# Kernel optimization log

Hardware: AMD Instinct MI355X
Metric: run time of the kernel (lower is better)

Reference implementation:

```python
import jax, jax.numpy as jnp
import numpy as np
from jax import lax

B, T, H, L, LAT, OUT, NH = 4096, 60, 512, 2, 128, 14, 4
EPS = 1e-5


def _ln(x, g, b):
    m = x.mean(-1, keepdims=True)
    v = ((x - m) ** 2).mean(-1, keepdims=True)
    return (x - m) / jnp.sqrt(v + EPS) * g + b


def setup_inputs() -> dict:
    key = jax.random.key(0)
    ks = jax.random.split(key, 24)
    f32 = jnp.float32
    def rn(k, shape, s=0.05):
        return jax.random.normal(k, shape, dtype=f32) * s
    return {
        'x': jax.random.normal(ks[0], (B, T, 17), dtype=f32),
        'conv1_w': rn(ks[1], (24, 9, 3)), 'conv1_b': rn(ks[2], (24,)),
        'bn1_g': jnp.ones(24, f32), 'bn1_b': jnp.zeros(24, f32),
        'bn1_rm': rn(ks[3], (24,), 0.1), 'bn1_rv': jnp.full((24,), 0.8, f32),
        'comp_w': rn(ks[4], (20, 8)), 'comp_b': rn(ks[5], (20,)),
        'proj_w': rn(ks[6], (H, 44)), 'proj_b': rn(ks[7], (H,)),
        'gates_w': rn(ks[8], (L, 5, H, 2 * H), 0.02), 'gates_b': rn(ks[9], (L, 5, H)),
        'retention': jnp.full((L, H), 0.9, f32),
        'expln_g': jnp.ones((L, H), f32), 'expln_b': jnp.zeros((L, H), f32),
        'ln_g': jnp.ones((L, H), f32), 'ln_b': jnp.zeros((L, H), f32),
        'attn_in_w': rn(ks[10], (3 * H, H), 0.02), 'attn_in_b': rn(ks[11], (3 * H,)),
        'attn_out_w': rn(ks[12], (H, H), 0.02), 'attn_out_b': rn(ks[13], (H,)),
        'bneck_w': rn(ks[14], (LAT, H)), 'bneck_b': rn(ks[15], (LAT,)),
        'bn2_g': jnp.ones(LAT, f32), 'bn2_b': jnp.zeros(LAT, f32),
        'bn2_rm': rn(ks[16], (LAT,), 0.1), 'bn2_rv': jnp.full((LAT,), 0.9, f32),
        'out_w': rn(ks[17], (OUT, LAT)), 'out_b': rn(ks[18], (OUT,)),
    }


def _forward(x, conv1_w, conv1_b, bn1_g, bn1_b, bn1_rm, bn1_rv, comp_w, comp_b,
             proj_w, proj_b, gates_w, gates_b, retention, expln_g, expln_b,
             ln_g, ln_b, attn_in_w, attn_in_b, attn_out_w, attn_out_b,
             bneck_w, bneck_b, bn2_g, bn2_b, bn2_rm, bn2_rv, out_w, out_b):
    bsz = x.shape[0]
    hd = proj_w.shape[0]
    nlayers = gates_w.shape[0]
    # --- conv branch on relative features (eval-mode BatchNorm) ---
    rel = x[:, :, :9].transpose(0, 2, 1)                      # [B,9,T]
    y = lax.conv_general_dilated(rel, conv1_w, (1,), [(1, 1)],
                                 dimension_numbers=('NCH', 'OIH', 'NCH'))
    y = jax.nn.relu(y + conv1_b[None, :, None])
    y = (y - bn1_rm[None, :, None]) / jnp.sqrt(bn1_rv + EPS)[None, :, None] \
        * bn1_g[None, :, None] + bn1_b[None, :, None]
    th = y.shape[2] // 2
    y = y[:, :, :th * 2].reshape(bsz, 24, th, 2).max(-1)      # MaxPool1d(2)
    rel_feat = y.transpose(0, 2, 1)                           # [B,30,24]
    # --- company embedding branch ---
    comp = jax.nn.relu(x[:, :30, 9:] @ comp_w.T + comp_b)     # [B,30,20]
    combined = jnp.concatenate([rel_feat, comp], -1) @ proj_w.T + proj_b  # [B,30,H]
    # --- stacked xLSTM over time ---
    h0 = jnp.zeros((nlayers, bsz, hd), x.dtype)
    c0 = jnp.zeros((nlayers, bsz, hd), x.dtype)
    def step(carry, x_t):
        h, c = carry
        inp = x_t
        hs, cs = [], []
        for l in range(nlayers):
            comb = jnp.concatenate([inp, h[l]], -1)           # [B,2H]
            g = jnp.einsum('bk,ghk->gbh', comb, gates_w[l]) + gates_b[l][:, None, :]
            f = jax.nn.sigmoid(g[0]); i = jax.nn.sigmoid(g[1])
            o = jax.nn.sigmoid(g[2]); cc = jnp.tanh(g[3]); m = jax.nn.sigmoid(g[4])
            r = retention[l]
            c_new = f * c[l] + i * cc
            c_new = c_new * r + (1 - r) * c[l]
            c_new = m * c_new + (1 - m) * c[l]
            o_exp = jax.nn.sigmoid(_ln(o, expln_g[l], expln_b[l]))  # exp(z)/(1+exp(z))
            h_new = _ln(o_exp * jnp.tanh(c_new), ln_g[l], ln_b[l])
            hs.append(h_new); cs.append(c_new)
            inp = h_new
        return (jnp.stack(hs), jnp.stack(cs)), inp
    _, seq = lax.scan(step, (h0, c0), combined.transpose(1, 0, 2))
    seq = seq.transpose(1, 0, 2)                              # [B,30,H]
    # --- multi-head self attention (eval, 4 heads) ---
    dh = hd // NH
    qkv = seq @ attn_in_w.T + attn_in_b
    q, k, v = jnp.split(qkv, 3, axis=-1)
    q = q.reshape(bsz, -1, NH, dh); k = k.reshape(bsz, -1, NH, dh); v = v.reshape(bsz, -1, NH, dh)
    scores = jnp.einsum('bqhd,bkhd->bhqk', q, k) / jnp.sqrt(jnp.float32(dh))
    attn = jnp.einsum('bhqk,bkhd->bqhd', jax.nn.softmax(scores, -1), v)
    attn = attn.reshape(bsz, -1, hd) @ attn_out_w.T + attn_out_b
    final = attn[:, -1, :]
    latent = final @ bneck_w.T + bneck_b
    latent = (latent - bn2_rm) / jnp.sqrt(bn2_rv + EPS) * bn2_g + bn2_b
    return latent @ out_w.T + out_b


def reference(x, conv1_w, conv1_b, bn1_g, bn1_b, bn1_rm, bn1_rv, comp_w, comp_b,
              proj_w, proj_b, gates_w, gates_b, retention, expln_g, expln_b,
              ln_g, ln_b, attn_in_w, attn_in_b, attn_out_w, attn_out_b,
              bneck_w, bneck_b, bn2_g, bn2_b, bn2_rm, bn2_rv, out_w, out_b):
    return _forward(x, conv1_w, conv1_b, bn1_g, bn1_b, bn1_rm, bn1_rv, comp_w, comp_b,
                    proj_w, proj_b, gates_w, gates_b, retention, expln_g, expln_b,
                    ln_g, ln_b, attn_in_w, attn_in_b, attn_out_w, attn_out_b,
                    bneck_w, bneck_b, bn2_g, bn2_b, bn2_rm, bn2_rv, out_w, out_b)
```

## Files before the change

kernel.cpp:

```cpp
#include <hip/hip_runtime.h>
#include <hip/hip_bf16.h>

#define B_   4096
#define T_   60
#define TT   30
#define H_   512
#define L_   2
#define NH_  4
#define DH_  128
#define LAT_ 128
#define OUT_ 14
#define NGATE_ (5*H_)
#define EPSF 1e-5f
#define FEATK 64
#define K0M  (FEATK + H_)

typedef __attribute__((ext_vector_type(8))) short bf16x8;
typedef __attribute__((ext_vector_type(4))) short bf16x4;
typedef __attribute__((ext_vector_type(4))) float f32x4;

__device__ __forceinline__ float sigmoidf_(float x) { return 1.0f / (1.0f + __expf(-x)); }
__device__ __forceinline__ float bf2f(short s) {
    return __uint_as_float(((unsigned)(unsigned short)s) << 16);
}

__device__ __forceinline__ void async_load16(const void* g, void* l) {
    __builtin_amdgcn_global_load_lds((const __attribute__((address_space(1))) void*)g,
                                     (__attribute__((address_space(3))) void*)l, 16, 0, 0);
}

__device__ __forceinline__ int perm_row(int n) {
    int g = n >> 9, j = n & 511;
    return (j >> 4) * 80 + g * 16 + (j & 15);
}

__global__ __launch_bounds__(256) void cvt_bf16(const float* __restrict__ in,
                                                __hip_bfloat16* __restrict__ out, long n) {
    long i = (long)blockIdx.x * blockDim.x + threadIdx.x;
    long stride = (long)gridDim.x * blockDim.x;
    for (; i < n; i += stride) out[i] = __float2bfloat16(in[i]);
}

__global__ __launch_bounds__(256) void zero_f32(float* __restrict__ p, long n) {
    long i = (long)blockIdx.x * blockDim.x + threadIdx.x;
    long stride = (long)gridDim.x * blockDim.x;
    for (; i < n; i += stride) p[i] = 0.0f;
}

__global__ __launch_bounds__(256)
void perm_w1(const float* __restrict__ gw, __hip_bfloat16* __restrict__ w1p) {
    long i = (long)blockIdx.x * 256 + threadIdx.x;
    if (i >= (long)NGATE_ * 2 * H_) return;
    int n = (int)(i >> 10), k = (int)(i & 1023);
    w1p[(long)perm_row(n) * (2 * H_) + k] = __float2bfloat16(gw[i]);
}

__global__ __launch_bounds__(256)
void build_w0m(const float* __restrict__ gw, const float* __restrict__ pw,
               const float* __restrict__ pb, const float* __restrict__ gb,
               __hip_bfloat16* __restrict__ w0p, float* __restrict__ bc) {
    const int tid = threadIdx.x;
    const int n = blockIdx.x * 4 + (tid >> 6);
    const int f = tid & 63;
    const long np = perm_row(n);
    const float* wrow = gw + (long)n * (2 * H_);
    float acc = 0.f;
    if (f < 44) {
        for (int k = 0; k < H_; ++k) acc += wrow[k] * pw[k * 44 + f];
    }
    w0p[np * K0M + f] = __float2bfloat16(acc);
    #pragma unroll
    for (int j = 0; j < 8; ++j) {
        int col = f * 8 + j;
        w0p[np * K0M + FEATK + col] = __float2bfloat16(wrow[H_ + col]);
    }
    float s = 0.f;
    #pragma unroll
    for (int j = 0; j < 8; ++j) s += wrow[f * 8 + j] * pb[f * 8 + j];
    #pragma unroll
    for (int off = 32; off > 0; off >>= 1) s += __shfl_down(s, off, 64);
    if (f == 0) bc[n] = gb[n] + s;
}

__global__ __launch_bounds__(256)
void build_wkd(const float* __restrict__ aiw, __hip_bfloat16* __restrict__ wkd) {
    int i = blockIdx.x * 256 + threadIdx.x;
    if (i >= 2048 * 512) return;
    int n = i >> 9, k = i & 511;
    float v = ((k >> 7) == (n >> 9)) ? aiw[(H_ + k) * H_ + (n & 511)] : 0.f;
    wkd[i] = __float2bfloat16(v);
}

__global__ __launch_bounds__(256)
void build_wvd(const float* __restrict__ aiw, __hip_bfloat16* __restrict__ wvd) {
    int i = blockIdx.x * 256 + threadIdx.x;
    if (i >= 512 * 2048) return;
    int n = i >> 11, k = i & 2047;
    float v = ((k >> 9) == (n >> 7)) ? aiw[(2 * H_ + n) * H_ + (k & 511)] : 0.f;
    wvd[i] = __float2bfloat16(v);
}

__global__ __launch_bounds__(256)
void frontend_kernel(const float* __restrict__ x,
                     const float* __restrict__ cw, const float* __restrict__ cb,
                     const float* __restrict__ bg, const float* __restrict__ bb,
                     const float* __restrict__ brm, const float* __restrict__ brv,
                     const float* __restrict__ compw, const float* __restrict__ compb,
                     __hip_bfloat16* __restrict__ feat_out) {
    const int b = blockIdx.x, tid = threadIdx.x;
    __shared__ float xs[T_ * 17];
    __shared__ float ybuf[24][T_];
    __shared__ float feat[TT][44];

    for (int i = tid; i < T_ * 17; i += 256) xs[i] = x[(long)b * T_ * 17 + i];
    __syncthreads();

    for (int i = tid; i < 24 * T_; i += 256) {
        int oc = i / T_, t = i % T_;
        float acc = cb[oc];
        #pragma unroll
        for (int kk = 0; kk < 3; ++kk) {
            int tt = t + kk - 1;
            if (tt >= 0 && tt < T_) {
                #pragma unroll
                for (int ic = 0; ic < 9; ++ic)
                    acc += xs[tt * 17 + ic] * cw[(oc * 9 + ic) * 3 + kk];
            }
        }
        acc = fmaxf(acc, 0.f);
        acc = (acc - brm[oc]) * rsqrtf(brv[oc] + EPSF) * bg[oc] + bb[oc];
        ybuf[oc][t] = acc;
    }
    __syncthreads();

    for (int i = tid; i < TT * 24; i += 256) {
        int u = i / 24, oc = i % 24;
        feat[u][oc] = fmaxf(ybuf[oc][2 * u], ybuf[oc][2 * u + 1]);
    }
    for (int i = tid; i < TT * 20; i += 256) {
        int u = i / 20, oc = i % 20;
        float acc = compb[oc];
        #pragma unroll
        for (int j = 0; j < 8; ++j) acc += xs[u * 17 + 9 + j] * compw[oc * 8 + j];
        feat[u][24 + oc] = fmaxf(acc, 0.f);
    }
    __syncthreads();

    for (int i = tid; i < TT * FEATK; i += 256) {
        int u = i >> 6, c = i & 63;
        float v = (c < 44) ? feat[u][c] : 0.f;
        feat_out[((long)b * TT + u) * FEATK + c] = __float2bfloat16(v);
    }
}

template <int WRITE_BF16>
__device__ __forceinline__
void gemm_core(const __hip_bfloat16* __restrict__ A0, int lda0,
               const __hip_bfloat16* __restrict__ A1, int lda1, int ksplit,
               const __hip_bfloat16* __restrict__ W, int ldw,
               const float* __restrict__ bias,
               void* __restrict__ Cout, int ldc, int K, int bx, int by) {
    __shared__ __hip_bfloat16 As[128 * 64];
    __shared__ __hip_bfloat16 Bs[128 * 64];
    const int tid = threadIdx.x;
    const int wave = tid >> 6, lane = tid & 63;
    const long m0 = (long)by * 128;
    const long n0 = (long)bx * 128;

    f32x4 acc[4][4] = {};

    for (int k0 = 0; k0 < K; k0 += 64) {
        __syncthreads();
        #pragma unroll
        for (int it = 0; it < 4; ++it) {
            int id = it * 256 + tid;
            int row = id >> 3;
            int kc = ((id & 7) ^ (row & 7)) << 3;
            int gk = k0 + kc;
            const __hip_bfloat16* srcA;
            if (gk < ksplit) srcA = A0 + (m0 + row) * (long)lda0 + gk;
            else             srcA = A1 + (m0 + row) * (long)lda1 + (gk - ksplit);
            async_load16(srcA, &As[id * 8]);
            const __hip_bfloat16* srcB = W + (n0 + row) * (long)ldw + gk;
            async_load16(srcB, &Bs[id * 8]);
        }
        __syncthreads();
        #pragma unroll
        for (int ks = 0; ks < 2; ++ks) {
            const int kb = ((ks * 4 + (lane >> 4)) ^ (lane & 7)) << 3;
            const int ar = (wave >> 1) * 64 + (lane & 15);
            const int br = (wave & 1) * 64 + (lane & 15);
            bf16x8 afr[4], bfr[4];
            #pragma unroll
            for (int i = 0; i < 4; ++i) afr[i] = *(const bf16x8*)&As[(ar + i * 16) * 64 + kb];
            #pragma unroll
            for (int i = 0; i < 4; ++i) bfr[i] = *(const bf16x8*)&Bs[(br + i * 16) * 64 + kb];
            #pragma unroll
            for (int mi = 0; mi < 4; ++mi)
                #pragma unroll
                for (int ni = 0; ni < 4; ++ni)
                    acc[mi][ni] = __builtin_amdgcn_mfma_f32_16x16x32_bf16(afr[mi], bfr[ni], acc[mi][ni], 0, 0, 0);
        }
    }

    const int cr = (lane >> 4) * 4;
    const int ccol = lane & 15;
    #pragma unroll
    for (int ni = 0; ni < 4; ++ni) {
        long col = n0 + (wave & 1) * 64 + ni * 16 + ccol;
        float bv = bias ? bias[col] : 0.f;
        #pragma unroll
        for (int mi = 0; mi < 4; ++mi) {
            long rowb = m0 + (wave >> 1) * 64 + mi * 16 + cr;
            #pragma unroll
            for (int r = 0; r < 4; ++r) {
                float v = acc[mi][ni][r] + bv;
                if (WRITE_BF16)
                    ((__hip_bfloat16*)Cout)[(rowb + r) * (long)ldc + col] = __float2bfloat16(v);
                else
                    ((float*)Cout)[(rowb + r) * (long)ldc + col] = v;
            }
        }
    }
}

template <int WRITE_BF16>
__global__ __launch_bounds__(256)
void gemm_bias(const __hip_bfloat16* __restrict__ A0, int lda0,
               const __hip_bfloat16* __restrict__ A1, int lda1, int ksplit,
               const __hip_bfloat16* __restrict__ W, int ldw,
               const float* __restrict__ bias,
               void* __restrict__ Cout, int ldc, int K) {
    gemm_core<WRITE_BF16>(A0, lda0, A1, lda1, ksplit, W, ldw, bias, Cout, ldc, K,
                          blockIdx.x, blockIdx.y);
}

__device__ __forceinline__
void fused_gate_core(const __hip_bfloat16* __restrict__ A0, int lda0,
                     const __hip_bfloat16* __restrict__ A1, int lda1,
                     int ksplit, int K,
                     const __hip_bfloat16* __restrict__ Wp, int ldw,
                     const float* __restrict__ bias,
                     const float* __restrict__ ret,
                     float* __restrict__ c_t,
                     float* __restrict__ opre,
                     float* __restrict__ tcn,
                     int m, int nblk) {
    __shared__ __hip_bfloat16 As[2][128 * 32];
    __shared__ __hip_bfloat16 Bs[2][80 * 32];
    const int tid = threadIdx.x;
    const int wave = tid >> 6, lane = tid & 63;
    const long m0 = (long)m * 128;
    const int n0row = nblk * 80;
    const int jbase = nblk * 16;

    f32x4 acc[2][5] = {};

    auto stage = [&](int hb, int k0) {
        #pragma unroll
        for (int it = 0; it < 2; ++it) {
            int sid = it * 256 + tid;
            int row = sid >> 2;
            int kc = ((sid & 3) ^ ((row >> 1) & 3)) << 3;
            int gk = k0 + kc;
            const __hip_bfloat16* srcA;
            if (gk < ksplit) srcA = A0 + (m0 + row) * (long)lda0 + gk;
            else             srcA = A1 + (m0 + row) * (long)lda1 + (gk - ksplit);
            async_load16(srcA, &As[hb][sid * 8]);
        }
        {
            int sid = tid;
            int row = sid >> 2;
            int kc = ((sid & 3) ^ ((row >> 1) & 3)) << 3;
            async_load16(Wp + (long)(n0row + row) * ldw + k0 + kc, &Bs[hb][sid * 8]);
        }
        if (tid < 64) {
            int sid = 256 + tid;
            int row = sid >> 2;
            int kc = ((sid & 3) ^ ((row >> 1) & 3)) << 3;
            async_load16(Wp + (long)(n0row + row) * ldw + k0 + kc, &Bs[hb][sid * 8]);
        }
    };

    stage(0, 0);
    const int nslab = K >> 5;
    const int kb = ((lane >> 4) ^ ((lane >> 1) & 3)) << 3;
    const int arb = wave * 32 + (lane & 15);
    const int brb = lane & 15;

    for (int kk = 0; kk < nslab; ++kk) {
        const int hb = kk & 1;
        __syncthreads();
        if (kk + 1 < nslab) stage(hb ^ 1, (kk + 1) << 5);
        bf16x8 afr[2], bfr[5];
        #pragma unroll
        for (int i = 0; i < 2; ++i) afr[i] = *(const bf16x8*)&As[hb][(arb + i * 16) * 32 + kb];
        #pragma unroll
        for (int i = 0; i < 5; ++i) bfr[i] = *(const bf16x8*)&Bs[hb][(brb + i * 16) * 32 + kb];
        #pragma unroll
        for (int mi = 0; mi < 2; ++mi)
            #pragma unroll
            for (int ni = 0; ni < 5; ++ni)
                acc[mi][ni] = __builtin_amdgcn_mfma_f32_16x16x32_bf16(bfr[ni], afr[mi], acc[mi][ni], 0, 0, 0);
    }

    const int q = lane >> 4;
    #pragma unroll
    for (int mi = 0; mi < 2; ++mi) {
        const long b = m0 + wave * 32 + mi * 16 + (lane & 15);
        f32x4 ov, tv;
        #pragma unroll
        for (int r = 0; r < 4; ++r) {
            const int jg = jbase + 4 * q + r;
            float f  = sigmoidf_(acc[mi][0][r] + bias[jg]);
            float ii = sigmoidf_(acc[mi][1][r] + bias[512 + jg]);
            float o  = sigmoidf_(acc[mi][2][r] + bias[1024 + jg]);
            float cc = tanhf(acc[mi][3][r] + bias[1536 + jg]);
            float mg = sigmoidf_(acc[mi][4][r] + bias[2048 + jg]);
            float cold = c_t[(long)jg * B_ + b];
            float rr = ret[jg];
            float cn = f * cold + ii * cc;
            cn = cn * rr + (1.f - rr) * cold;
            cn = mg * cn + (1.f - mg) * cold;
            c_t[(long)jg * B_ + b] = cn;
            ov[r] = o;
            tv[r] = tanhf(cn);
        }
        *(f32x4*)&opre[b * H_ + jbase + 4 * q] = ov;
        *(f32x4*)&tcn [b * H_ + jbase + 4 * q] = tv;
    }
}

__global__ __launch_bounds__(256)
void fused_gate_single(const __hip_bfloat16* A0, int lda0, const __hip_bfloat16* A1,
                       int lda1, int ksplit, int K,
                       const __hip_bfloat16* Wp, int ldw,
                       const float* bias, const float* ret, float* c_t,
                       float* opre, float* tcn) {
    const int id = blockIdx.x;
    const int xcd = id & 7;
    const int rest = id >> 3;
    const int m = xcd * 4 + (rest & 3);
    const int n = (rest >> 2) & 31;
    fused_gate_core(A0, lda0, A1, lda1, ksplit, K, Wp, ldw, bias, ret, c_t,
                    opre, tcn, m, n);
}

__global__ __launch_bounds__(256)
void fused_gate_dual(const __hip_bfloat16* A0a, int lda0a, const __hip_bfloat16* A1a,
                     int lda1a, int ksplita, int Ka,
                     const __hip_bfloat16* Wpa, int ldwa,
                     const float* biasa, const float* reta, float* cta,
                     float* oprea, float* tcna,
                     const __hip_bfloat16* A0b, int lda0b, const __hip_bfloat16* A1b,
                     int lda1b, int ksplitb, int Kb,
                     const __hip_bfloat16* Wpb, int ldwb,
                     const float* biasb, const float* retb, float* ctb,
                     float* opreb, float* tcnb) {
    const int id = blockIdx.x;
    const int xcd = id & 7;
    const int rest = id >> 3;
    const int m = xcd * 4 + (rest & 3);
    const int n = (rest >> 2) & 31;
    const int z = rest >> 7;
    if (z == 0)
        fused_gate_core(A0a, lda0a, A1a, lda1a, ksplita, Ka, Wpa, ldwa,
                        biasa, reta, cta, oprea, tcna, m, n);
    else
        fused_gate_core(A0b, lda0b, A1b, lda1b, ksplitb, Kb, Wpb, ldwb,
                        biasb, retb, ctb, opreb, tcnb, m, n);
}

__device__ __forceinline__ void block_reduce2(float& a, float& b, float* red) {
    #pragma unroll
    for (int off = 32; off > 0; off >>= 1) {
        a += __shfl_down(a, off, 64);
        b += __shfl_down(b, off, 64);
    }
    int lane = threadIdx.x & 63, w = threadIdx.x >> 6;
    if (lane == 0) { red[w] = a; red[8 + w] = b; }
    __syncthreads();
    a = red[0] + red[1] + red[2] + red[3];
    b = red[8] + red[9] + red[10] + red[11];
    __syncthreads();
}

__device__ __forceinline__
void gate_ln_body(const float* __restrict__ opre,
                  const float* __restrict__ tcn,
                  const float* __restrict__ elg, const float* __restrict__ elb,
                  const float* __restrict__ lng, const float* __restrict__ lnb,
                  __hip_bfloat16* __restrict__ hout, long hstride, int b) {
    const int tid = threadIdx.x;
    __shared__ float red[16];

    float o_[2], t_[2];
    float s = 0.f, s2 = 0.f;
    #pragma unroll
    for (int u = 0; u < 2; ++u) {
        int j = tid + u * 256;
        float o = opre[(long)b * H_ + j];
        float t = tcn[(long)b * H_ + j];
        o_[u] = o; t_[u] = t;
        s += o; s2 += o * o;
    }
    block_reduce2(s, s2, red);
    float mean = s * (1.f / H_);
    float var = s2 * (1.f / H_) - mean * mean;
    float rstd = rsqrtf(var + EPSF);

    float val[2];
    float s3 = 0.f, s4 = 0.f;
    #pragma unroll
    for (int u = 0; u < 2; ++u) {
        int j = tid + u * 256;
        float on = (o_[u] - mean) * rstd * elg[j] + elb[j];
        float v = sigmoidf_(on) * t_[u];
        val[u] = v; s3 += v; s4 += v * v;
    }
    block_reduce2(s3, s4, red);
    float mean2 = s3 * (1.f / H_);
    float var2 = s4 * (1.f / H_) - mean2 * mean2;
    float rstd2 = rsqrtf(var2 + EPSF);
    #pragma unroll
    for (int u = 0; u < 2; ++u) {
        int j = tid + u * 256;
        float h = (val[u] - mean2) * rstd2 * lng[j] + lnb[j];
        hout[(long)b * hstride + j] = __float2bfloat16(h);
    }
}

__global__ __launch_bounds__(256)
void gate_ln(const float* __restrict__ opre,
             const float* __restrict__ tcn,
             const float* __restrict__ elg, const float* __restrict__ elb,
             const float* __restrict__ lng, const float* __restrict__ lnb,
             __hip_bfloat16* __restrict__ hout, long hstride) {
    gate_ln_body(opre, tcn, elg, elb, lng, lnb, hout, hstride, blockIdx.x);
}

__global__ __launch_bounds__(256)
void gate_ln_dual(const float* oa, const float* ta,
                  const float* elga, const float* elba,
                  const float* lnga, const float* lnba,
                  __hip_bfloat16* houta, long hstridea,
                  const float* ob, const float* tb,
                  const float* elgb, const float* elbb,
                  const float* lngb, const float* lnbb,
                  __hip_bfloat16* houtb, long hstrideb) {
    int bid = blockIdx.x;
    bool isB = bid >= B_;
    int b = isB ? bid - B_ : bid;
    gate_ln_body(isB ? ob : oa, isB ? tb : ta,
                 isB ? elgb : elga, isB ? elbb : elba,
                 isB ? lngb : lnga, isB ? lnbb : lnba,
                 isB ? houtb : houta, isB ? hstrideb : hstridea, b);
}

__global__ __launch_bounds__(256)
void attn_fused(const __hip_bfloat16* __restrict__ seq,
                const __hip_bfloat16* __restrict__ U,
                __hip_bfloat16* __restrict__ sbar) {
    const int b = blockIdx.x, tid = threadIdx.x;
    const int h = tid >> 6, lane = tid & 63;
    const int c0 = lane * 8;
    __shared__ float ps[NH_ * TT];
    const float scale = 0.08838834764831845f;

    float uq[8];
    {
        bf16x8 uv = *(const bf16x8*)&U[(size_t)b * (NH_ * H_) + h * H_ + c0];
        for (int j = 0; j < 8; ++j) uq[j] = bf2f(uv[j]);
    }
    const __hip_bfloat16* srow = seq + (size_t)b * TT * H_;

    for (int t = 0; t < TT; ++t) {
        bf16x8 sv = *(const bf16x8*)&srow[t * H_ + c0];
        float a = 0.f;
        for (int j = 0; j < 8; ++j) a += uq[j] * bf2f(sv[j]);
        a += __shfl_xor(a, 32);
        a += __shfl_xor(a, 16);
        a += __shfl_xor(a, 8);
        a += __shfl_xor(a, 4);
        a += __shfl_xor(a, 2);
        a += __shfl_xor(a, 1);
        if (lane == 0) ps[h * TT + t] = a * scale;
    }
    __syncthreads();

    float mx = -1e30f;
    for (int t = 0; t < TT; ++t) mx = fmaxf(mx, ps[h * TT + t]);
    float den = 0.f;
    for (int t = 0; t < TT; ++t) den += __expf(ps[h * TT + t] - mx);
    float inv = 1.f / den;

    float accv[8];
    for (int j = 0; j < 8; ++j) accv[j] = 0.f;
    for (int t = 0; t < TT; ++t) {
        float w = __expf(ps[h * TT + t] - mx) * inv;
        bf16x8 sv = *(const bf16x8*)&srow[t * H_ + c0];
        for (int j = 0; j < 8; ++j) accv[j] += w * bf2f(sv[j]);
    }
    bf16x8 outv;
    for (int j = 0; j < 8; ++j) {
        __hip_bfloat16 hv = __float2bfloat16(accv[j]);
        outv[j] = *(short*)&hv;
    }
    *(bf16x8*)&sbar[(size_t)b * (NH_ * H_) + h * H_ + c0] = outv;
}

__global__ __launch_bounds__(128)
void head_kernel(const float* __restrict__ lat_in,
                 const float* __restrict__ g2, const float* __restrict__ b2,
                 const float* __restrict__ rm2, const float* __restrict__ rv2,
                 const float* __restrict__ ow, const float* __restrict__ ob,
                 float* __restrict__ out) {
    const int b = blockIdx.x, tid = threadIdx.x;
    __shared__ float ls[LAT_];
    float a = lat_in[(long)b * LAT_ + tid];
    ls[tid] = (a - rm2[tid]) * rsqrtf(rv2[tid] + EPSF) * g2[tid] + b2[tid];
    __syncthreads();
    if (tid < OUT_) {
        float acc = ob[tid];
        #pragma unroll 4
        for (int j = 0; j < LAT_; ++j) acc += ls[j] * ow[tid * LAT_ + j];
        out[(long)b * OUT_ + tid] = acc;
    }
}

extern "C" void kernel_launch(void* const* d_in, const int* in_sizes, int n_in,
                              void* d_out, int out_size, void* d_ws, size_t ws_size,
                              hipStream_t stream) {
    const float* x        = (const float*)d_in[0];
    const float* conv1_w  = (const float*)d_in[1];
    const float* conv1_b  = (const float*)d_in[2];
    const float* bn1_g    = (const float*)d_in[3];
    const float* bn1_b    = (const float*)d_in[4];
    const float* bn1_rm   = (const float*)d_in[5];
    const float* bn1_rv   = (const float*)d_in[6];
    const float* comp_w   = (const float*)d_in[7];
    const float* comp_b   = (const float*)d_in[8];
    const float* proj_w   = (const float*)d_in[9];
    const float* proj_b   = (const float*)d_in[10];
    const float* gates_w  = (const float*)d_in[11];
    const float* gates_b  = (const float*)d_in[12];
    const float* retention= (const float*)d_in[13];
    const float* expln_g  = (const float*)d_in[14];
    const float* expln_b  = (const float*)d_in[15];
    const float* ln_g     = (const float*)d_in[16];
    const float* ln_b     = (const float*)d_in[17];
    const float* attn_in_w  = (const float*)d_in[18];
    const float* attn_in_b  = (const float*)d_in[19];
    const float* attn_out_w = (const float*)d_in[20];
    const float* attn_out_b = (const float*)d_in[21];
    const float* bneck_w  = (const float*)d_in[22];
    const float* bneck_b  = (const float*)d_in[23];
    const float* bn2_g    = (const float*)d_in[24];
    const float* bn2_b    = (const float*)d_in[25];
    const float* bn2_rm   = (const float*)d_in[26];
    const float* bn2_rv   = (const float*)d_in[27];
    const float* out_w    = (const float*)d_in[28];
    const float* out_b    = (const float*)d_in[29];
    float* out = (float*)d_out;

    char* base = (char*)d_ws;
    size_t off = 0;
    auto alloc = [&](size_t nbytes) -> char* {
        char* p = base + off;
        off += (nbytes + 255) & ~(size_t)255;
        return p;
    };
    __hip_bfloat16* seq_bf = (__hip_bfloat16*)alloc((size_t)B_ * TT * H_ * 2);
    size_t g_bytes = (size_t)B_ * NGATE_ * 2;
    char* un = alloc(2 * g_bytes);
    float* opreA = (float*)un;
    float* tcnA  = (float*)(un + (size_t)8 * 1024 * 1024);
    float* opreB = (float*)(un + (size_t)16 * 1024 * 1024);
    float* tcnB  = (float*)(un + (size_t)24 * 1024 * 1024);
    __hip_bfloat16* U_bf    = (__hip_bfloat16*)un;
    __hip_bfloat16* sbar_bf = (__hip_bfloat16*)(un + (size_t)16 * 1024 * 1024);
    __hip_bfloat16* wkd_bf  = (__hip_bfloat16*)(un + (size_t)32 * 1024 * 1024);
    __hip_bfloat16* wvd_bf  = (__hip_bfloat16*)(un + (size_t)35 * 1024 * 1024);
    __hip_bfloat16* feat_bf = (__hip_bfloat16*)alloc((size_t)B_ * TT * FEATK * 2);
    float*          c0t   = (float*)alloc((size_t)B_ * H_ * 4);
    float*          c1t   = (float*)alloc((size_t)B_ * H_ * 4);
    __hip_bfloat16* h0_bf = (__hip_bfloat16*)alloc((size_t)B_ * H_ * 2);
    __hip_bfloat16* q_bf  = (__hip_bfloat16*)alloc((size_t)B_ * H_ * 2);
    __hip_bfloat16* fin_bf = q_bf;
    __hip_bfloat16* av_bf = (__hip_bfloat16*)alloc((size_t)B_ * H_ * 2);
    float*          lat_f = (float*)alloc((size_t)B_ * LAT_ * 4);
    __hip_bfloat16* w1p_bf = (__hip_bfloat16*)alloc((size_t)NGATE_ * 2 * H_ * 2);
    __hip_bfloat16* w0p_bf = (__hip_bfloat16*)alloc((size_t)NGATE_ * K0M * 2);
    float*          bc_f  = (float*)alloc((size_t)NGATE_ * 4);
    __hip_bfloat16* ai_bf = (__hip_bfloat16*)alloc((size_t)H_ * H_ * 2);
    __hip_bfloat16* ao_bf = (__hip_bfloat16*)alloc((size_t)H_ * H_ * 2);
    __hip_bfloat16* bw_bf = (__hip_bfloat16*)alloc((size_t)LAT_ * H_ * 2);
    (void)ws_size; (void)in_sizes; (void)n_in; (void)out_size;

    const int WL = 5 * H_ * 2 * H_;
    perm_w1<<<(NGATE_ * 2 * H_) / 256, 256, 0, stream>>>(gates_w + WL, w1p_bf);
    build_w0m<<<NGATE_ / 4, 256, 0, stream>>>(gates_w, proj_w, proj_b, gates_b,
                                              w0p_bf, bc_f);
    cvt_bf16<<<256, 256, 0, stream>>>(attn_in_w, ai_bf, (long)H_ * H_);
    cvt_bf16<<<256, 256, 0, stream>>>(attn_out_w, ao_bf, (long)H_ * H_);
    cvt_bf16<<<64, 256, 0, stream>>>(bneck_w, bw_bf, (long)LAT_ * H_);
    zero_f32<<<2048, 256, 0, stream>>>(c0t, (long)2 * B_ * H_);

    frontend_kernel<<<B_, 256, 0, stream>>>(x, conv1_w, conv1_b, bn1_g, bn1_b, bn1_rm,
                                            bn1_rv, comp_w, comp_b, feat_bf);

    fused_gate_single<<<1024, 256, 0, stream>>>(
        feat_bf, TT * FEATK, (const __hip_bfloat16*)nullptr, 0, FEATK, FEATK,
        w0p_bf, K0M, bc_f, retention, c0t, opreB, tcnB);
    gate_ln<<<B_, 256, 0, stream>>>(opreB, tcnB, expln_g, expln_b,
                                    ln_g, ln_b, h0_bf, H_);

    for (int t = 0; t < TT - 1; ++t) {
        fused_gate_dual<<<2048, 256, 0, stream>>>(
            h0_bf, H_, (t == 0) ? (const __hip_bfloat16*)nullptr
                                : seq_bf + (size_t)(t - 1) * H_,
            TT * H_, H_, (t == 0) ? H_ : 2 * H_,
            w1p_bf, 2 * H_, gates_b + NGATE_, retention + H_, c1t, opreA, tcnA,
            feat_bf + (size_t)(t + 1) * FEATK, TT * FEATK, h0_bf, H_, FEATK, K0M,
            w0p_bf, K0M, bc_f, retention, c0t, opreB, tcnB);
        gate_ln_dual<<<2 * B_, 256, 0, stream>>>(
            opreA, tcnA, expln_g + H_, expln_b + H_, ln_g + H_, ln_b + H_,
            seq_bf + (size_t)t * H_, TT * H_,
            opreB, tcnB, expln_g, expln_b, ln_g, ln_b, h0_bf, H_);
    }
    fused_gate_single<<<1024, 256, 0, stream>>>(
        h0_bf, H_, seq_bf + (size_t)(TT - 2) * H_, TT * H_, H_, 2 * H_,
        w1p_bf, 2 * H_, gates_b + NGATE_, retention + H_, c1t, opreA, tcnA);
    gate_ln<<<B_, 256, 0, stream>>>(opreA, tcnA, expln_g + H_, expln_b + H_,
                                    ln_g + H_, ln_b + H_,
                                    seq_bf + (size_t)(TT - 1) * H_, TT * H_);

    build_wkd<<<4096, 256, 0, stream>>>(attn_in_w, wkd_bf);
    build_wvd<<<4096, 256, 0, stream>>>(attn_in_w, wvd_bf);

    gemm_bias<1><<<dim3(H_ / 128, B_ / 128), 256, 0, stream>>>(
        seq_bf + (size_t)29 * H_, TT * H_, (const __hip_bfloat16*)nullptr, 0, H_,
        ai_bf, H_, attn_in_b, (void*)q_bf, H_, H_);

    gemm_bias<1><<<dim3(2048 / 128, B_ / 128), 256, 0, stream>>>(
        q_bf, H_, (const __hip_bfloat16*)nullptr, 0, H_,
        wkd_bf, H_, (const float*)nullptr, (void*)U_bf, 2048, H_);

    attn_fused<<<B_, 256, 0, stream>>>(seq_bf, U_bf, sbar_bf);

    gemm_bias<1><<<dim3(H_ / 128, B_ / 128), 256, 0, stream>>>(
        sbar_bf, 2048, (const __hip_bfloat16*)nullptr, 0, 2048,
        wvd_bf, 2048, attn_in_b + 2 * H_, (void*)av_bf, H_, 2048);

    gemm_bias<1><<<dim3(H_ / 128, B_ / 128), 256, 0, stream>>>(
        av_bf, H_, (const __hip_bfloat16*)nullptr, 0, H_,
        ao_bf, H_, attn_out_b, (void*)fin_bf, H_, H_);

    gemm_bias<0><<<dim3(LAT_ / 128, B_ / 128), 256, 0, stream>>>(
        fin_bf, H_, (const __hip_bfloat16*)nullptr, 0, H_,
        bw_bf, H_, bneck_b, (void*)lat_f, LAT_, H_);
    head_kernel<<<B_, 128, 0, stream>>>(lat_f, bn2_g, bn2_b, bn2_rm, bn2_rv,
                                        out_w, out_b, out);
}
```

Before: 2.666 ms.

## Load gate GEMM operands directly from global memory per wave instead of LDS staging

Removes the double-buffered shared-memory staging and per-slab block barriers in the fused gate GEMM. Each wave now reads its A and W fragments straight from global memory into registers and splits the K loop into two phases, one per input source. This drops LDS traffic and __syncthreads. In exchange, the W tile is no longer shared through LDS, so each of the 4 waves fetches it separately, and the loads are uncoalesced 16-byte strided reads that rely on cache.

```diff
diff --git a/kernel.cpp b/kernel.cpp
--- a/kernel.cpp
+++ b/kernel.cpp
@@ -236,6 +236,27 @@
 }
 
 __device__ __forceinline__
+void wave_gemm_phase(const __hip_bfloat16* __restrict__ ap, long lda,
+                     const __hip_bfloat16* __restrict__ wp, long ldw,
+                     int nslab, f32x4 (&acc)[2][5]) {
+    #pragma unroll 4
+    for (int s = 0; s < nslab; ++s) {
+        bf16x8 afr[2], bfr[5];
+        #pragma unroll
+        for (int mi = 0; mi < 2; ++mi)
+            afr[mi] = *(const bf16x8*)(ap + (long)mi * 16 * lda + (long)s * 32);
+        #pragma unroll
+        for (int ni = 0; ni < 5; ++ni)
+            bfr[ni] = *(const bf16x8*)(wp + (long)ni * 16 * ldw + (long)s * 32);
+        #pragma unroll
+        for (int mi = 0; mi < 2; ++mi)
+            #pragma unroll
+            for (int ni = 0; ni < 5; ++ni)
+                acc[mi][ni] = __builtin_amdgcn_mfma_f32_16x16x32_bf16(bfr[ni], afr[mi], acc[mi][ni], 0, 0, 0);
+    }
+}
+
+__device__ __forceinline__
 void fused_gate_core(const __hip_bfloat16* __restrict__ A0, int lda0,
                      const __hip_bfloat16* __restrict__ A1, int lda1,
                      int ksplit, int K,
@@ -246,68 +267,28 @@
                      float* __restrict__ opre,
                      float* __restrict__ tcn,
                      int m, int nblk) {
-    __shared__ __hip_bfloat16 As[2][128 * 32];
-    __shared__ __hip_bfloat16 Bs[2][80 * 32];
     const int tid = threadIdx.x;
     const int wave = tid >> 6, lane = tid & 63;
     const long m0 = (long)m * 128;
     const int n0row = nblk * 80;
     const int jbase = nblk * 16;
+    const int rsel = lane & 15;
+    const int kchunk = (lane >> 4) * 8;
 
     f32x4 acc[2][5] = {};
-
-    auto stage = [&](int hb, int k0) {
-        #pragma unroll
-        for (int it = 0; it < 2; ++it) {
-            int sid = it * 256 + tid;
-            int row = sid >> 2;
-            int kc = ((sid & 3) ^ ((row >> 1) & 3)) << 3;
-            int gk = k0 + kc;
-            const __hip_bfloat16* srcA;
-            if (gk < ksplit) srcA = A0 + (m0 + row) * (long)lda0 + gk;
-            else             srcA = A1 + (m0 + row) * (long)lda1 + (gk - ksplit);
-            async_load16(srcA, &As[hb][sid * 8]);
-        }
-        {
-            int sid = tid;
-            int row = sid >> 2;
-            int kc = ((sid & 3) ^ ((row >> 1) & 3)) << 3;
-            async_load16(Wp + (long)(n0row + row) * ldw + k0 + kc, &Bs[hb][sid * 8]);
-        }
-        if (tid < 64) {
-            int sid = 256 + tid;
-            int row = sid >> 2;
-            int kc = ((sid & 3) ^ ((row >> 1) & 3)) << 3;
-            async_load16(Wp + (long)(n0row + row) * ldw + k0 + kc, &Bs[hb][sid * 8]);
-        }
-    };
-
-    stage(0, 0);
-    const int nslab = K >> 5;
-    const int kb = ((lane >> 4) ^ ((lane >> 1) & 3)) << 3;
-    const int arb = wave * 32 + (lane & 15);
-    const int brb = lane & 15;
-
-    for (int kk = 0; kk < nslab; ++kk) {
-        const int hb = kk & 1;
-        __syncthreads();
-        if (kk + 1 < nslab) stage(hb ^ 1, (kk + 1) << 5);
-        bf16x8 afr[2], bfr[5];
-        #pragma unroll
-        for (int i = 0; i < 2; ++i) afr[i] = *(const bf16x8*)&As[hb][(arb + i * 16) * 32 + kb];
-        #pragma unroll
-        for (int i = 0; i < 5; ++i) bfr[i] = *(const bf16x8*)&Bs[hb][(brb + i * 16) * 32 + kb];
-        #pragma unroll
-        for (int mi = 0; mi < 2; ++mi)
-            #pragma unroll
-            for (int ni = 0; ni < 5; ++ni)
-                acc[mi][ni] = __builtin_amdgcn_mfma_f32_16x16x32_bf16(bfr[ni], afr[mi], acc[mi][ni], 0, 0, 0);
-    }
+    const long arow = m0 + wave * 32 + rsel;
+    const __hip_bfloat16* wp = Wp + (long)(n0row + rsel) * ldw + kchunk;
+
+    wave_gemm_phase(A0 + arow * (long)lda0 + kchunk, lda0, wp, ldw,
+                    ksplit >> 5, acc);
+    if (K > ksplit)
+        wave_gemm_phase(A1 + arow * (long)lda1 + kchunk, lda1, wp + ksplit, ldw,
+                        (K - ksplit) >> 5, acc);
 
     const int q = lane >> 4;
     #pragma unroll
     for (int mi = 0; mi < 2; ++mi) {
-        const long b = m0 + wave * 32 + mi * 16 + (lane & 15);
+        const long b = m0 + wave * 32 + mi * 16 + rsel;
         f32x4 ov, tv;
         #pragma unroll
         for (int r = 0; r < 4; ++r) {
```

Measured after the change: 5.594 ms. 110% more time.

## Double gate GEMM N-tile to 160 with 2x2 wave layout and precomputed load pointers

Applied to the files above, without the earlier changes.

The fused gate GEMM tile grows from 128x80 to 128x160. The four waves are arranged 2x2, each computing 64 rows by 80 columns (4x5 MFMA accumulators), so each A tile is reused across twice as many output columns. Global load addresses are precomputed once outside the k-loop, and the A0/A1 split is decided per slab rather than per element. The grid is halved to 512 and 1024 blocks, which raises register and LDS use per block and may lower occupancy and wave count per CU.

```diff
diff --git a/kernel.cpp b/kernel.cpp
--- a/kernel.cpp
+++ b/kernel.cpp
@@ -247,67 +247,91 @@
                      float* __restrict__ tcn,
                      int m, int nblk) {
     __shared__ __hip_bfloat16 As[2][128 * 32];
-    __shared__ __hip_bfloat16 Bs[2][80 * 32];
+    __shared__ __hip_bfloat16 Bs[2][160 * 32];
     const int tid = threadIdx.x;
     const int wave = tid >> 6, lane = tid & 63;
+    const int wavem = wave >> 1, waven = wave & 1;
     const long m0 = (long)m * 128;
-    const int n0row = nblk * 80;
-    const int jbase = nblk * 16;
-
-    f32x4 acc[2][5] = {};
-
-    auto stage = [&](int hb, int k0) {
-        #pragma unroll
-        for (int it = 0; it < 2; ++it) {
-            int sid = it * 256 + tid;
-            int row = sid >> 2;
-            int kc = ((sid & 3) ^ ((row >> 1) & 3)) << 3;
-            int gk = k0 + kc;
-            const __hip_bfloat16* srcA;
-            if (gk < ksplit) srcA = A0 + (m0 + row) * (long)lda0 + gk;
-            else             srcA = A1 + (m0 + row) * (long)lda1 + (gk - ksplit);
-            async_load16(srcA, &As[hb][sid * 8]);
+    const int n0row = nblk * 160;
+    const int rsel = lane & 15;
+
+    const __hip_bfloat16* pA0[2];
+    const __hip_bfloat16* pA1[2];
+    int ldsA[2];
+    #pragma unroll
+    for (int it = 0; it < 2; ++it) {
+        int sid = it * 256 + tid;
+        int row = sid >> 2;
+        int kc = ((sid & 3) ^ ((row >> 1) & 3)) << 3;
+        ldsA[it] = sid * 8;
+        pA0[it] = A0 + (m0 + row) * (long)lda0 + kc;
+        pA1[it] = A1 ? (A1 + (m0 + row) * (long)lda1 + kc - ksplit) : pA0[it];
+    }
+    const __hip_bfloat16* pB[3];
+    int ldsB[3];
+    #pragma unroll
+    for (int it = 0; it < 2; ++it) {
+        int sid = it * 256 + tid;
+        int row = sid >> 2;
+        int kc = ((sid & 3) ^ ((row >> 1) & 3)) << 3;
+        ldsB[it] = sid * 8;
+        pB[it] = Wp + (long)(n0row + row) * ldw + kc;
+    }
+    {
+        int sid = 512 + tid;
+        int row = sid >> 2;
+        int kc = ((sid & 3) ^ ((row >> 1) & 3)) << 3;
+        ldsB[2] = sid * 8;
+        pB[2] = Wp + (long)(n0row + row) * ldw + kc;
+    }
+    const int ks_slab = ksplit >> 5;
+    const int nslab = K >> 5;
+
+    auto stage = [&](int hb, int kk) {
+        const long koff = (long)kk * 32;
+        if (kk < ks_slab) {
+            #pragma unroll
+            for (int it = 0; it < 2; ++it)
+                async_load16(pA0[it] + koff, &As[hb][ldsA[it]]);
+        } else {
+            #pragma unroll
+            for (int it = 0; it < 2; ++it)
+                async_load16(pA1[it] + koff, &As[hb][ldsA[it]]);
         }
-        {
-            int sid = tid;
-            int row = sid >> 2;
-            int kc = ((sid & 3) ^ ((row >> 1) & 3)) << 3;
-            async_load16(Wp + (long)(n0row + row) * ldw + k0 + kc, &Bs[hb][sid * 8]);
-        }
-        if (tid < 64) {
-            int sid = 256 + tid;
-            int row = sid >> 2;
-            int kc = ((sid & 3) ^ ((row >> 1) & 3)) << 3;
-            async_load16(Wp + (long)(n0row + row) * ldw + k0 + kc, &Bs[hb][sid * 8]);
-        }
+        #pragma unroll
+        for (int it = 0; it < 2; ++it)
+            async_load16(pB[it] + koff, &Bs[hb][ldsB[it]]);
+        if (tid < 128)
+            async_load16(pB[2] + koff, &Bs[hb][ldsB[2]]);
     };
 
     stage(0, 0);
-    const int nslab = K >> 5;
     const int kb = ((lane >> 4) ^ ((lane >> 1) & 3)) << 3;
-    const int arb = wave * 32 + (lane & 15);
-    const int brb = lane & 15;
+    f32x4 acc[4][5] = {};
 
     for (int kk = 0; kk < nslab; ++kk) {
         const int hb = kk & 1;
         __syncthreads();
-        if (kk + 1 < nslab) stage(hb ^ 1, (kk + 1) << 5);
-        bf16x8 afr[2], bfr[5];
-        #pragma unroll
-        for (int i = 0; i < 2; ++i) afr[i] = *(const bf16x8*)&As[hb][(arb + i * 16) * 32 + kb];
-        #pragma unroll
-        for (int i = 0; i < 5; ++i) bfr[i] = *(const bf16x8*)&Bs[hb][(brb + i * 16) * 32 + kb];
-        #pragma unroll
-        for (int mi = 0; mi < 2; ++mi)
+        if (kk + 1 < nslab) stage(hb ^ 1, kk + 1);
+        bf16x8 afr[4], bfr[5];
+        #pragma unroll
+        for (int i = 0; i < 4; ++i)
+            afr[i] = *(const bf16x8*)&As[hb][(wavem * 64 + i * 16 + rsel) * 32 + kb];
+        #pragma unroll
+        for (int i = 0; i < 5; ++i)
+            bfr[i] = *(const bf16x8*)&Bs[hb][(waven * 80 + i * 16 + rsel) * 32 + kb];
+        #pragma unroll
+        for (int mi = 0; mi < 4; ++mi)
             #pragma unroll
             for (int ni = 0; ni < 5; ++ni)
                 acc[mi][ni] = __builtin_amdgcn_mfma_f32_16x16x32_bf16(bfr[ni], afr[mi], acc[mi][ni], 0, 0, 0);
     }
 
     const int q = lane >> 4;
-    #pragma unroll
-    for (int mi = 0; mi < 2; ++mi) {
-        const long b = m0 + wave * 32 + mi * 16 + (lane & 15);
+    const int jbase = (nblk * 2 + waven) * 16;
+    #pragma unroll
+    for (int mi = 0; mi < 4; ++mi) {
+        const long b = m0 + wavem * 64 + mi * 16 + rsel;
         f32x4 ov, tv;
         #pragma unroll
         for (int r = 0; r < 4; ++r) {
@@ -341,7 +365,7 @@
     const int xcd = id & 7;
     const int rest = id >> 3;
     const int m = xcd * 4 + (rest & 3);
-    const int n = (rest >> 2) & 31;
+    const int n = (rest >> 2) & 15;
     fused_gate_core(A0, lda0, A1, lda1, ksplit, K, Wp, ldw, bias, ret, c_t,
                     opre, tcn, m, n);
 }
@@ -361,8 +385,8 @@
     const int xcd = id & 7;
     const int rest = id >> 3;
     const int m = xcd * 4 + (rest & 3);
-    const int n = (rest >> 2) & 31;
-    const int z = rest >> 7;
+    const int n = (rest >> 2) & 15;
+    const int z = rest >> 6;
     if (z == 0)
         fused_gate_core(A0a, lda0a, A1a, lda1a, ksplita, Ka, Wpa, ldwa,
                         biasa, reta, cta, oprea, tcna, m, n);
@@ -609,14 +633,14 @@
     frontend_kernel<<<B_, 256, 0, stream>>>(x, conv1_w, conv1_b, bn1_g, bn1_b, bn1_rm,
                                             bn1_rv, comp_w, comp_b, feat_bf);
 
-    fused_gate_single<<<1024, 256, 0, stream>>>(
+    fused_gate_single<<<512, 256, 0, stream>>>(
         feat_bf, TT * FEATK, (const __hip_bfloat16*)nullptr, 0, FEATK, FEATK,
         w0p_bf, K0M, bc_f, retention, c0t, opreB, tcnB);
     gate_ln<<<B_, 256, 0, stream>>>(opreB, tcnB, expln_g, expln_b,
                                     ln_g, ln_b, h0_bf, H_);
 
     for (int t = 0; t < TT - 1; ++t) {
-        fused_gate_dual<<<2048, 256, 0, stream>>>(
+        fused_gate_dual<<<1024, 256, 0, stream>>>(
             h0_bf, H_, (t == 0) ? (const __hip_bfloat16*)nullptr
                                 : seq_bf + (size_t)(t - 1) * H_,
             TT * H_, H_, (t == 0) ? H_ : 2 * H_,
@@ -628,7 +652,7 @@
             seq_bf + (size_t)t * H_, TT * H_,
             opreB, tcnB, expln_g, expln_b, ln_g, ln_b, h0_bf, H_);
     }
-    fused_gate_single<<<1024, 256, 0, stream>>>(
+    fused_gate_single<<<512, 256, 0, stream>>>(
         h0_bf, H_, seq_bf + (size_t)(TT - 2) * H_, TT * H_, H_, 2 * H_,
         w1p_bf, 2 * H_, gates_b + NGATE_, retention + H_, c1t, opreA, tcnA);
     gate_ln<<<B_, 256, 0, stream>>>(opreA, tcnA, expln_g + H_, expln_b + H_,
```

After: 2.635 ms. About the same (-1.2%).
